# Kernel tuning notes

Measured on AMD Instinct MI355X. Metric: run time of the kernel, lower is better.

Reference implementation:

```python
import jax, jax.numpy as jnp
import numpy as np

Q_LEN = 2048
K_LEN = 2048
BATCH = 2
EMBED = 1024
HEADS = 16
HEAD_DIM = EMBED // HEADS
PE_ROWS = 2 * K_LEN


def _shift(p):
    # Transformer-XL pad/flatten shift: p is [B, H, Q, S] with S = 2*K-1 -> [B, H, Q, K]
    B, H, Q, S = p.shape
    pp = jnp.pad(p, ((0, 0), (0, 0), (0, 1), (0, 1)))          # [B,H,Q+1,S+1]
    flat = pp.reshape(B, H, (Q + 1) * (S + 1))
    flat = jax.lax.slice_in_dim(flat, S // 2, S // 2 + Q * S, axis=-1)
    return flat.reshape(B, H, Q, S)[..., : (S + 1) // 2]


def setup_inputs() -> dict:
    key = jax.random.key(0)
    ks = jax.random.split(key, 11)
    ws = 0.02  # weight scale
    inp = {
        "query": jax.random.normal(ks[0], (Q_LEN, BATCH, EMBED), jnp.float32),
        "key": jax.random.normal(ks[1], (K_LEN, BATCH, EMBED), jnp.float32),
        "value": jax.random.normal(ks[2], (K_LEN, BATCH, EMBED), jnp.float32),
        "pe": jax.random.normal(ks[3], (PE_ROWS, EMBED), jnp.float32),
        "w_q": jax.random.normal(ks[4], (EMBED, EMBED), jnp.float32) * ws,
        "w_k": jax.random.normal(ks[5], (EMBED, EMBED), jnp.float32) * ws,
        "w_v": jax.random.normal(ks[6], (EMBED, EMBED), jnp.float32) * ws,
        "w_k_pos": jax.random.normal(ks[7], (EMBED, EMBED), jnp.float32) * ws,
        "out_proj": jax.random.normal(ks[8], (EMBED, EMBED), jnp.float32) * ws,
        "content_bias": jax.random.normal(ks[9], (HEADS, HEAD_DIM), jnp.float32) * ws,
        "pos_bias": jax.random.normal(ks[10], (HEADS, HEAD_DIM), jnp.float32) * ws,
        "attn_mask": jnp.triu(jnp.ones((Q_LEN, K_LEN), dtype=bool), k=1),  # causal
    }
    return inp


def reference(query, key, value, pe, w_q, w_k, w_v, w_k_pos, out_proj,
              content_bias, pos_bias, attn_mask):
    Qlen, B, E = query.shape
    Klen = key.shape[0]
    H, D = content_bias.shape
    scaling = D ** -0.5

    # projections (torch Linear: x @ W^T); layout -> [B, H, L, D]
    q = (query @ w_q.T).reshape(Qlen, B, H, D).transpose(1, 2, 0, 3)
    k = (key @ w_k.T).reshape(Klen, B, H, D).transpose(1, 2, 0, 3)
    v = (value @ w_v.T).reshape(Klen, B, H, D).transpose(1, 2, 0, 3)

    # relative position keys: pe slice of size 2K-1 starting at pe.size(0)//2 - K + 1
    lower = pe.shape[0] // 2 - Klen + 1
    pe_slice = jax.lax.dynamic_slice_in_dim(pe, lower, 2 * Klen - 1, axis=0)
    k_pos = (pe_slice @ w_k_pos.T).reshape(2 * Klen - 1, H, D).transpose(1, 0, 2)  # [H, 2K-1, D]

    content = jnp.einsum('bhqd,bhkd->bhqk', q + content_bias[None, :, None, :], k)
    pos = jnp.einsum('bhqd,hsd->bhqs', q + pos_bias[None, :, None, :], k_pos)
    pos = _shift(pos)  # [B, H, Q, K]

    attn = (content + pos) * scaling
    attn = jnp.where(attn_mask[None, None], -jnp.inf, attn)
    w = jax.nn.softmax(attn, axis=-1)

    out = jnp.einsum('bhqk,bhkd->bhqd', w, v)
    out = out.transpose(2, 0, 1, 3).reshape(Qlen, B, E)
    return out @ out_proj.T
```

## Files before the change

### kernel.cpp

```cpp
#include <hip/hip_runtime.h>
#include <hip/hip_bf16.h>

typedef __hip_bfloat16 bf16;
typedef __attribute__((ext_vector_type(8))) short short8;
typedef __attribute__((ext_vector_type(8))) unsigned short u16x8;
typedef __attribute__((ext_vector_type(4))) float f32x4;

#define QL   2048
#define KLEN 2048
#define BATCH 2
#define EMB  1024
#define NH   16
#define HD   64
#define SPE  4095

__device__ __forceinline__ int detect_f32_wave(const void* __restrict__ p) {
    const ushort4 v = ((const ushort4*)p)[threadIdx.x & 63];
    int c = 0;
    c += __popcll(__ballot(((v.x >> 7) & 0xFF) >= 0x8A));
    c += __popcll(__ballot(((v.y >> 7) & 0xFF) >= 0x8A));
    c += __popcll(__ballot(((v.z >> 7) & 0xFF) >= 0x8A));
    c += __popcll(__ballot(((v.w >> 7) & 0xFF) >= 0x8A));
    return c >= 8;
}

__device__ __forceinline__ ushort4 cvt4(const void* src, long u4i, int f32) {
    ushort4 o;
    if (f32) {
        float4 v = ((const float4*)src)[u4i];
        bf16 a = (bf16)v.x, b = (bf16)v.y, c = (bf16)v.z, e = (bf16)v.w;
        o.x = *(unsigned short*)&a; o.y = *(unsigned short*)&b;
        o.z = *(unsigned short*)&c; o.w = *(unsigned short*)&e;
    } else {
        o = ((const ushort4*)src)[u4i];
    }
    return o;
}

__global__ __launch_bounds__(256) void conv_w(
    const void* w0, const void* w1, const void* w2, const void* w3, const void* w4,
    const void* cb, const void* pb, bf16* __restrict__ wdst)
{
    const int t = threadIdx.x;
    const int bid = blockIdx.x;
    __shared__ int f32s;
    if (bid < 1280) {
        const int seg = bid >> 8, inner = bid & 255;
        const void* src = seg == 0 ? w0 : seg == 1 ? w1 : seg == 2 ? w2 : seg == 3 ? w3 : w4;
        bf16* d = wdst + (size_t)seg * 1048576;
        if (t < 64) { int r = detect_f32_wave(src); if (t == 0) f32s = r; }
        __syncthreads();
        const int f32 = f32s;
#pragma unroll
        for (int i = 0; i < 4; i++) {
            long u4i = (long)inner * 1024 + i * 256 + t;
            ((ushort4*)d)[u4i] = cvt4(src, u4i, f32);
        }
    } else {
        if (t < 64) { int r = detect_f32_wave(cb); if (t == 0) f32s = r; }
        __syncthreads();
        const int f32 = f32s;
        ((ushort4*)(wdst + 5242880))[t]        = cvt4(cb, t, f32);
        ((ushort4*)(wdst + 5242880 + 1024))[t] = cvt4(pb, t, f32);
    }
}

__device__ __forceinline__ void llds16(const bf16* g, bf16* l) {
    __builtin_amdgcn_global_load_lds(
        (const __attribute__((address_space(1))) void*)g,
        (__attribute__((address_space(3))) void*)l,
        16, 0, 0);
}

__device__ __forceinline__ short8 pack_f32x8(const float4& a, const float4& b) {
    short8 o; bf16 x;
    x = (bf16)a.x; o[0] = *(short*)&x;  x = (bf16)a.y; o[1] = *(short*)&x;
    x = (bf16)a.z; o[2] = *(short*)&x;  x = (bf16)a.w; o[3] = *(short*)&x;
    x = (bf16)b.x; o[4] = *(short*)&x;  x = (bf16)b.y; o[5] = *(short*)&x;
    x = (bf16)b.z; o[6] = *(short*)&x;  x = (bf16)b.w; o[7] = *(short*)&x;
    return o;
}

template<bool F32>
__device__ void gloop64(
    const void* Av, const bf16* W, int m0, int n0, int mode,
    bf16* Asd, bf16* Wsd,
    int t, int wm, int wn, int lm, int quad, f32x4 acc[2][4])
{
    long go[2];
#pragma unroll
    for (int i = 0; i < 2; i++) {
        int c = i * 256 + t, r = c >> 3, gc = (c & 7) ^ (r & 7);
        int ar = m0 + r;
        if (mode == 3) { ar = ar + 1; if (ar > 4095) ar = 4095; }
        go[i] = (long)ar * 1024 + gc * 8;
    }

#pragma unroll 1
    for (int k0 = 0; k0 < 1024; k0 += 64) {
        u16x8 au[2]; float4 a32[2][2];
#pragma unroll
        for (int i = 0; i < 2; i++) {
            long e = go[i] + k0;
            if (F32) {
                const float4* F = (const float4*)Av;
                a32[i][0] = F[e >> 2];
                a32[i][1] = F[(e >> 2) + 1];
            } else {
                au[i] = ((const u16x8*)Av)[e >> 3];
            }
        }
#pragma unroll
        for (int i = 0; i < 4; i++) {
            int c = i * 256 + t, r = c >> 3, gc = (c & 7) ^ (r & 7);
            llds16(W + (size_t)(n0 + r) * 1024 + k0 + gc * 8, Wsd + (c & ~63) * 8);
        }
        asm volatile("s_waitcnt vmcnt(0)" ::: "memory");
#pragma unroll
        for (int i = 0; i < 2; i++) {
            int c = i * 256 + t;
            short8 v;
            if (F32) v = pack_f32x8(a32[i][0], a32[i][1]);
            else     v = *(short8*)&au[i];
            *(short8*)&Asd[c * 8] = v;
        }
        asm volatile("s_waitcnt lgkmcnt(0)" ::: "memory");
        __builtin_amdgcn_s_barrier();
        __builtin_amdgcn_sched_barrier(0);

#pragma unroll
        for (int kk = 0; kk < 2; kk++) {
            short8 af[2], wf[4];
#pragma unroll
            for (int x = 0; x < 2; x++) {
                int ra = wm + x * 16 + lm;
                af[x] = *(const short8*)&Asd[ra * 64 + (((kk * 4 + quad) ^ (ra & 7)) * 8)];
            }
#pragma unroll
            for (int y = 0; y < 4; y++) {
                int rb = wn + y * 16 + lm;
                wf[y] = *(const short8*)&Wsd[rb * 64 + (((kk * 4 + quad) ^ (rb & 7)) * 8)];
            }
#pragma unroll
            for (int mt = 0; mt < 2; mt++)
#pragma unroll
                for (int nt = 0; nt < 4; nt++)
                    acc[mt][nt] = __builtin_amdgcn_mfma_f32_16x16x32_bf16(
                        af[mt], wf[nt], acc[mt][nt], 0, 0, 0);
        }
        __builtin_amdgcn_s_barrier();
    }
}

__global__ __launch_bounds__(256) void gemm_big(
    const void* __restrict__ Aq, const void* __restrict__ Ak,
    const void* __restrict__ Avv, const void* __restrict__ Ape,
    const bf16* __restrict__ ao, const bf16* __restrict__ wslab,
    bf16* __restrict__ qc, bf16* __restrict__ qp,
    bf16* __restrict__ kw, bf16* __restrict__ vw,
    bf16* __restrict__ kpos, float* __restrict__ outf, int mode_base)
{
    const int nwg = gridDim.x;
    const int d = blockIdx.x;
    const int g = (d & 7) * (nwg >> 3) + (d >> 3);
    const int by = g & 7;
    const int bx = (g >> 3) & 63;
    const int bz = g >> 9;

    const int mode = mode_base + bz;
    const void* A = mode == 0 ? Aq : mode == 1 ? Ak : mode == 2 ? Avv :
                    mode == 3 ? Ape : (const void*)ao;
    const bf16* W = wslab + (size_t)mode * 1048576;

    __shared__ __align__(16) bf16 Asd[64 * 64];
    __shared__ __align__(16) bf16 Wsd[128 * 64];
    __shared__ int f32s;

    const int t = threadIdx.x;
    const int w = t >> 6, lane = t & 63, lm = lane & 15, quad = lane >> 4;
    const int m0 = bx * 64, n0 = by * 128;
    const int wm = (w & 1) * 32, wn = (w >> 1) * 64;

    if (t < 64) { int r = detect_f32_wave(A); if (t == 0) f32s = r; }
    __syncthreads();

    f32x4 acc[2][4] = {};

    if (f32s) gloop64<true >(A, W, m0, n0, mode, Asd, Wsd, t, wm, wn, lm, quad, acc);
    else      gloop64<false>(A, W, m0, n0, mode, Asd, Wsd, t, wm, wn, lm, quad, acc);

    const bf16* cbb = wslab + 5242880;
    const bf16* pbb = wslab + 5242880 + 1024;

#pragma unroll
    for (int mt = 0; mt < 2; mt++) {
#pragma unroll
        for (int nt = 0; nt < 4; nt++) {
#pragma unroll
            for (int r4 = 0; r4 < 4; r4++) {
                int row = m0 + wm + mt * 16 + quad * 4 + r4;
                int col = n0 + wn + nt * 16 + lm;
                float v = acc[mt][nt][r4];
                if (mode == 0) {
                    int l = row >> 1, b = row & 1;
                    int h = col >> 6, dd = col & 63;
                    size_t idx = ((size_t)(b * NH + h) * QL + l) * HD + dd;
                    qc[idx] = (bf16)(v + __bfloat162float(cbb[col]));
                    qp[idx] = (bf16)(v + __bfloat162float(pbb[col]));
                } else if (mode == 1) {
                    int l = row >> 1, b = row & 1;
                    int h = col >> 6, dd = col & 63;
                    kw[((size_t)(b * NH + h) * KLEN + l) * HD + dd] = (bf16)v;
                } else if (mode == 2) {
                    int l = row >> 1, b = row & 1;
                    int h = col >> 6, dd = col & 63;
                    vw[((size_t)(b * NH + h) * KLEN + l) * HD + dd] = (bf16)v;
                } else if (mode == 3) {
                    if (row < SPE) {
                        int h = col >> 6, dd = col & 63;
                        kpos[((size_t)h * SPE + row) * HD + dd] = (bf16)v;
                    }
                } else {
                    outf[(size_t)row * 1024 + col] = v;
                }
            }
        }
    }
}

#define NEG_INF (-1.0e30f)
#define SCL2 0.18033688011f

__global__ __launch_bounds__(256) void attn_mfma(
    const bf16* __restrict__ qc_g, const bf16* __restrict__ qp_g,
    const bf16* __restrict__ k_g,  const bf16* __restrict__ v_g,
    const bf16* __restrict__ kpos_g, bf16* __restrict__ ao)
{
    const int lin = blockIdx.x + (blockIdx.y << 6) + (blockIdx.z << 10);
    const int xcd = lin & 7, s = lin >> 3;
    const int g   = (xcd << 2) | (s >> 6);
    const int u   = s & 63;
    const int bx  = 63 - u;
    const int h   = g & 15;
    const int b   = g >> 4;
    const int q0  = bx * 32;

    const bf16* qc_bh  = qc_g + ((size_t)(b * NH + h) * QL) * HD;
    const bf16* qp_bh  = qp_g + ((size_t)(b * NH + h) * QL) * HD;
    const bf16* k_bh   = k_g  + ((size_t)(b * NH + h) * KLEN) * HD;
    const bf16* v_bh   = v_g  + ((size_t)(b * NH + h) * KLEN) * HD;
    const bf16* kpos_h = kpos_g + (size_t)h * SPE * HD;

    __shared__ __align__(16) bf16 K_s [64 * 64];
    __shared__ __align__(16) bf16 Kp_s[96 * 64];
    __shared__ __align__(16) bf16 Vt_s[64 * 64];
    __shared__ __align__(16) bf16 Pb_s[32 * 64];
    __shared__ float Sc_s[32][69];
    __shared__ float Pt_s[32][98];
    __shared__ float arow_s[32];

    const int t = threadIdx.x;
    const int w = t >> 6, lane = t & 63, lm = lane & 15, quad = lane >> 4;

    const int sr = t >> 3;
    const int sc = (t & 7) * 8;
    const int vrr = t >> 3, vch = t & 7;
    const int vkc = vrr >> 2;

    const int mtc = w & 1;
    const int ntc = (w >> 1) * 2;
    const int mtp = w >> 1;
    const int ntp = (w & 1) * 3;

    float m_run = NEG_INF, l_part = 0.0f;
    f32x4 accO[2] = {{0,0,0,0},{0,0,0,0}};
    u16x8 vv0, vv1;

    const int nkt = (bx >> 1) + 1;

    short8 aQc0, aQc1, aQp0, aQp1;
    {
        const bf16* qr = qc_bh + (size_t)(q0 + mtc * 16 + lm) * HD;
        aQc0 = *(const short8*)(qr + quad * 8);
        aQc1 = *(const short8*)(qr + (4 + quad) * 8);
        const bf16* pr = qp_bh + (size_t)(q0 + mtp * 16 + lm) * HD;
        aQp0 = *(const short8*)(pr + quad * 8);
        aQp1 = *(const short8*)(pr + (4 + quad) * 8);
    }

#pragma unroll
    for (int i = 0; i < 2; i++) {
        int c = i * 256 + t, r = c >> 3, ch = c & 7, gc = ch ^ (r & 7);
        llds16(k_bh + (size_t)r * HD + gc * 8, K_s + (c & ~63) * 8);
    }
    {
        const int s0 = 2016 - q0;
#pragma unroll
        for (int i = 0; i < 3; i++) {
            int c = i * 256 + t, r = c >> 3, ch = c & 7, gc = ch ^ (r & 7);
            llds16(kpos_h + (size_t)(s0 + r) * HD + gc * 8, Kp_s + (c & ~63) * 8);
        }
    }
    vv0 = *(const u16x8*)&v_bh[(size_t)(2 * vrr)     * HD + vch * 8];
    vv1 = *(const u16x8*)&v_bh[(size_t)(2 * vrr + 1) * HD + vch * 8];

    for (int kt = 0; kt < nkt; kt++) {
        const int k0 = kt * 64;

        __syncthreads();

        {
            const int off = (2 * vrr) & 7;
#pragma unroll
            for (int j = 0; j < 8; j++) {
                unsigned int pair = (unsigned int)vv0[j] | ((unsigned int)vv1[j] << 16);
                int slot = vkc ^ vch ^ j;
                *(unsigned int*)&Vt_s[(vch * 8 + j) * 64 + slot * 8 + off] = pair;
            }
        }

        {
#pragma unroll
            for (int n = 0; n < 2; n++) {
                int rowB = (ntc + n) * 16 + lm;
                short8 b0 = *(const short8*)&K_s[rowB * 64 + ((quad)     ^ (rowB & 7)) * 8];
                short8 b1 = *(const short8*)&K_s[rowB * 64 + ((4 + quad) ^ (rowB & 7)) * 8];
                f32x4 acc = {0, 0, 0, 0};
                acc = __builtin_amdgcn_mfma_f32_16x16x32_bf16(aQc0, b0, acc, 0, 0, 0);
                acc = __builtin_amdgcn_mfma_f32_16x16x32_bf16(aQc1, b1, acc, 0, 0, 0);
#pragma unroll
                for (int r = 0; r < 4; r++)
                    Sc_s[mtc * 16 + quad * 4 + r][(ntc + n) * 16 + lm] = acc[r];
            }
        }
        {
#pragma unroll
            for (int n = 0; n < 3; n++) {
                int rowB = (ntp + n) * 16 + lm;
                short8 b0 = *(const short8*)&Kp_s[rowB * 64 + ((quad)     ^ (rowB & 7)) * 8];
                short8 b1 = *(const short8*)&Kp_s[rowB * 64 + ((4 + quad) ^ (rowB & 7)) * 8];
                f32x4 acc = {0, 0, 0, 0};
                acc = __builtin_amdgcn_mfma_f32_16x16x32_bf16(aQp0, b0, acc, 0, 0, 0);
                acc = __builtin_amdgcn_mfma_f32_16x16x32_bf16(aQp1, b1, acc, 0, 0, 0);
#pragma unroll
                for (int r = 0; r < 4; r++)
                    Pt_s[mtp * 16 + quad * 4 + r][(ntp + n) * 16 + lm] = acc[r];
            }
        }

        __syncthreads();

        if (kt + 1 < nkt) {
            const int k0n = k0 + 64;
            const int s0n = k0n - q0 + 2016;
#pragma unroll
            for (int i = 0; i < 2; i++) {
                int c = i * 256 + t, r = c >> 3, ch = c & 7, gc = ch ^ (r & 7);
                llds16(k_bh + (size_t)(k0n + r) * HD + gc * 8, K_s + (c & ~63) * 8);
            }
#pragma unroll
            for (int i = 0; i < 3; i++) {
                int c = i * 256 + t, r = c >> 3, ch = c & 7, gc = ch ^ (r & 7);
                llds16(kpos_h + (size_t)(s0n + r) * HD + gc * 8, Kp_s + (c & ~63) * 8);
            }
            vv0 = *(const u16x8*)&v_bh[(size_t)(k0n + 2 * vrr)     * HD + vch * 8];
            vv1 = *(const u16x8*)&v_bh[(size_t)(k0n + 2 * vrr + 1) * HD + vch * 8];
        }

        {
            float p[8];
            float pmax = NEG_INF;
#pragma unroll
            for (int j = 0; j < 8; j++) {
                int col = sc + j;
                float sv = (Sc_s[sr][col] + Pt_s[sr][col - sr + 31]) * SCL2;
                if (k0 + col > q0 + sr) sv = NEG_INF;
                p[j] = sv;
                pmax = fmaxf(pmax, sv);
            }
            float alpha = 1.0f;
            if (!__all(pmax <= m_run + 11.5f)) {
                float mx = pmax;
                mx = fmaxf(mx, __shfl_xor(mx, 1, 8));
                mx = fmaxf(mx, __shfl_xor(mx, 2, 8));
                mx = fmaxf(mx, __shfl_xor(mx, 4, 8));
                float mnew = fmaxf(m_run, mx);
                alpha = __builtin_amdgcn_exp2f(m_run - mnew);
                m_run = mnew;
            }
            float ls = 0.0f;
#pragma unroll
            for (int j = 0; j < 8; j++) {
                p[j] = __builtin_amdgcn_exp2f(p[j] - m_run);
                ls += p[j];
            }
            l_part = l_part * alpha + ls;
            if ((t & 7) == 0) arow_s[sr] = alpha;
            short8 pv;
#pragma unroll
            for (int j = 0; j < 8; j++) { bf16 x = (bf16)p[j]; pv[j] = *(short*)&x; }
            *(short8*)&Pb_s[sr * 64 + ((t & 7) ^ (sr & 7)) * 8] = pv;
        }

        asm volatile("s_waitcnt lgkmcnt(0)" ::: "memory");
        __builtin_amdgcn_s_barrier();
        __builtin_amdgcn_sched_barrier(0);

        {
            float al[4];
#pragma unroll
            for (int r = 0; r < 4; r++) al[r] = arow_s[mtc * 16 + quad * 4 + r];
            int rowA = mtc * 16 + lm;
            short8 a0 = *(const short8*)&Pb_s[rowA * 64 + ((quad)     ^ (rowA & 7)) * 8];
            short8 a1 = *(const short8*)&Pb_s[rowA * 64 + ((4 + quad) ^ (rowA & 7)) * 8];
#pragma unroll
            for (int n = 0; n < 2; n++) {
                int d = (ntc + n) * 16 + lm;
                int ds = (d >> 3) ^ (d & 7);
                short8 b0 = *(const short8*)&Vt_s[d * 64 + ((quad     ^ ds)) * 8];
                short8 b1 = *(const short8*)&Vt_s[d * 64 + (((4 + quad) ^ ds)) * 8];
#pragma unroll
                for (int r = 0; r < 4; r++) accO[n][r] *= al[r];
                accO[n] = __builtin_amdgcn_mfma_f32_16x16x32_bf16(a0, b0, accO[n], 0, 0, 0);
                accO[n] = __builtin_amdgcn_mfma_f32_16x16x32_bf16(a1, b1, accO[n], 0, 0, 0);
            }
        }
    }

    l_part += __shfl_xor(l_part, 1, 8);
    l_part += __shfl_xor(l_part, 2, 8);
    l_part += __shfl_xor(l_part, 4, 8);

    __syncthreads();
    if ((t & 7) == 0) arow_s[sr] = l_part;
    __syncthreads();

    float linv[4];
#pragma unroll
    for (int r = 0; r < 4; r++) linv[r] = 1.0f / arow_s[mtc * 16 + quad * 4 + r];
#pragma unroll
    for (int n = 0; n < 2; n++) {
#pragma unroll
        for (int r = 0; r < 4; r++) {
            int row = mtc * 16 + quad * 4 + r;
            ao[(((size_t)(q0 + row) * BATCH + b) * EMB) + h * HD + (ntc + n) * 16 + lm] =
                (bf16)(accO[n][r] * linv[r]);
        }
    }
}

extern "C" void kernel_launch(void* const* d_in, const int* in_sizes, int n_in,
                              void* d_out, int out_size, void* d_ws, size_t ws_size,
                              hipStream_t stream)
{
    const void* query = d_in[0];
    const void* key   = d_in[1];
    const void* value = d_in[2];
    const void* pe    = d_in[3];
    const void* w_q   = d_in[4];
    const void* w_k   = d_in[5];
    const void* w_v   = d_in[6];
    const void* w_kp  = d_in[7];
    const void* w_out = d_in[8];
    const void* cb    = d_in[9];
    const void* pb    = d_in[10];
    float* out = (float*)d_out;

    const size_t SLAB = 4194304;
    bf16* qc   = (bf16*)d_ws;
    bf16* qp   = qc + SLAB;
    bf16* kw   = qp + SLAB;
    bf16* vw   = kw + SLAB;
    bf16* kpos = vw + SLAB;
    bf16* ao   = kpos + SLAB;
    bf16* wqb  = ao + SLAB;

    dim3 blk(256);

    conv_w<<<dim3(1281), blk, 0, stream>>>(w_q, w_k, w_v, w_kp, w_out, cb, pb, wqb);

    gemm_big<<<dim3(2048), blk, 0, stream>>>(
        query, key, value, pe, nullptr, wqb, qc, qp, kw, vw, kpos, nullptr, 0);

    attn_mfma<<<dim3(64, NH, BATCH), blk, 0, stream>>>(qc, qp, kw, vw, kpos, ao);

    gemm_big<<<dim3(512), blk, 0, stream>>>(
        query, key, value, pe, ao, wqb, qc, qp, kw, vw, kpos, out, 4);
}
```

Before: 344.7 us.

## Double-buffer weight tiles and prefetch next A tile in projection GEMM

The projection GEMM loop now double-buffers the W tile in LDS and issues the global loads for the next A and W tiles right after the barrier, so they overlap the current tile's MFMA work. Each wave also computes the fp32-detection flag itself instead of going through a shared variable and an extra __syncthreads. This adds LDS usage (a second 16KB W buffer) and more live registers for the prefetched A data, which may lower occupancy.

```diff
diff --git a/kernel.cpp b/kernel.cpp
--- a/kernel.cpp
+++ b/kernel.cpp
@@ -43,23 +43,18 @@
 {
     const int t = threadIdx.x;
     const int bid = blockIdx.x;
-    __shared__ int f32s;
     if (bid < 1280) {
         const int seg = bid >> 8, inner = bid & 255;
         const void* src = seg == 0 ? w0 : seg == 1 ? w1 : seg == 2 ? w2 : seg == 3 ? w3 : w4;
         bf16* d = wdst + (size_t)seg * 1048576;
-        if (t < 64) { int r = detect_f32_wave(src); if (t == 0) f32s = r; }
-        __syncthreads();
-        const int f32 = f32s;
+        const int f32 = detect_f32_wave(src);
 #pragma unroll
         for (int i = 0; i < 4; i++) {
             long u4i = (long)inner * 1024 + i * 256 + t;
             ((ushort4*)d)[u4i] = cvt4(src, u4i, f32);
         }
     } else {
-        if (t < 64) { int r = detect_f32_wave(cb); if (t == 0) f32s = r; }
-        __syncthreads();
-        const int f32 = f32s;
+        const int f32 = detect_f32_wave(cb);
         ((ushort4*)(wdst + 5242880))[t]        = cvt4(cb, t, f32);
         ((ushort4*)(wdst + 5242880 + 1024))[t] = cvt4(pb, t, f32);
     }
@@ -96,9 +91,10 @@
         go[i] = (long)ar * 1024 + gc * 8;
     }
 
-#pragma unroll 1
-    for (int k0 = 0; k0 < 1024; k0 += 64) {
-        u16x8 au[2]; float4 a32[2][2];
+    u16x8 auA[2], auB[2];
+    float4 fA[2][2], fB[2][2];
+
+    auto loadA = [&](int k0, u16x8 au[2], float4 a32[2][2]) {
 #pragma unroll
         for (int i = 0; i < 2; i++) {
             long e = go[i] + k0;
@@ -110,12 +106,8 @@
                 au[i] = ((const u16x8*)Av)[e >> 3];
             }
         }
-#pragma unroll
-        for (int i = 0; i < 4; i++) {
-            int c = i * 256 + t, r = c >> 3, gc = (c & 7) ^ (r & 7);
-            llds16(W + (size_t)(n0 + r) * 1024 + k0 + gc * 8, Wsd + (c & ~63) * 8);
-        }
-        asm volatile("s_waitcnt vmcnt(0)" ::: "memory");
+    };
+    auto writeA = [&](u16x8 au[2], float4 a32[2][2]) {
 #pragma unroll
         for (int i = 0; i < 2; i++) {
             int c = i * 256 + t;
@@ -124,10 +116,36 @@
             else     v = *(short8*)&au[i];
             *(short8*)&Asd[c * 8] = v;
         }
+    };
+    auto stageW = [&](bf16* dst, int k0) {
+#pragma unroll
+        for (int i = 0; i < 4; i++) {
+            int c = i * 256 + t, r = c >> 3, gc = (c & 7) ^ (r & 7);
+            llds16(W + (size_t)(n0 + r) * 1024 + k0 + gc * 8, dst + (c & ~63) * 8);
+        }
+    };
+
+    loadA(0, auA, fA);
+    stageW(Wsd, 0);
+
+#pragma unroll 1
+    for (int it = 0; it < 16; ++it) {
+        const int k0 = it * 64;
+        bf16* Wc = Wsd + (it & 1) * (128 * 64);
+        bf16* Wn = Wsd + ((it + 1) & 1) * (128 * 64);
+
+        asm volatile("s_waitcnt vmcnt(0)" ::: "memory");
+        if (it & 1) writeA(auB, fB); else writeA(auA, fA);
         asm volatile("s_waitcnt lgkmcnt(0)" ::: "memory");
         __builtin_amdgcn_s_barrier();
         __builtin_amdgcn_sched_barrier(0);
 
+        if (it + 1 < 16) {
+            if (it & 1) loadA(k0 + 64, auA, fA);
+            else        loadA(k0 + 64, auB, fB);
+            stageW(Wn, k0 + 64);
+        }
+
 #pragma unroll
         for (int kk = 0; kk < 2; kk++) {
             short8 af[2], wf[4];
@@ -139,7 +157,7 @@
 #pragma unroll
             for (int y = 0; y < 4; y++) {
                 int rb = wn + y * 16 + lm;
-                wf[y] = *(const short8*)&Wsd[rb * 64 + (((kk * 4 + quad) ^ (rb & 7)) * 8)];
+                wf[y] = *(const short8*)&Wc[rb * 64 + (((kk * 4 + quad) ^ (rb & 7)) * 8)];
             }
 #pragma unroll
             for (int mt = 0; mt < 2; mt++)
@@ -173,21 +191,19 @@
     const bf16* W = wslab + (size_t)mode * 1048576;
 
     __shared__ __align__(16) bf16 Asd[64 * 64];
-    __shared__ __align__(16) bf16 Wsd[128 * 64];
-    __shared__ int f32s;
+    __shared__ __align__(16) bf16 Wsd[2][128 * 64];
 
     const int t = threadIdx.x;
     const int w = t >> 6, lane = t & 63, lm = lane & 15, quad = lane >> 4;
     const int m0 = bx * 64, n0 = by * 128;
     const int wm = (w & 1) * 32, wn = (w >> 1) * 64;
 
-    if (t < 64) { int r = detect_f32_wave(A); if (t == 0) f32s = r; }
-    __syncthreads();
+    const int f32 = detect_f32_wave(A);
 
     f32x4 acc[2][4] = {};
 
-    if (f32s) gloop64<true >(A, W, m0, n0, mode, Asd, Wsd, t, wm, wn, lm, quad, acc);
-    else      gloop64<false>(A, W, m0, n0, mode, Asd, Wsd, t, wm, wn, lm, quad, acc);
+    if (f32) gloop64<true >(A, W, m0, n0, mode, Asd, &Wsd[0][0], t, wm, wn, lm, quad, acc);
+    else     gloop64<false>(A, W, m0, n0, mode, Asd, &Wsd[0][0], t, wm, wn, lm, quad, acc);
 
     const bf16* cbb = wslab + 5242880;
     const bf16* pbb = wslab + 5242880 + 1024;
```

New measurement: 363.4 us. +5.4%, slower.
